# Kernel tuning notes

Hardware: AMD Instinct MI355X
Metric: run time of the kernel (lower is better)

Reference implementation:

```python
import jax, jax.numpy as jnp
import numpy as np


def setup_inputs() -> dict:
    key = jax.random.key(0)
    x = jax.random.normal(key, (8192, 16384), dtype=jnp.float32)
    return {"x": x, "k": 128}


def reference(x, k):
    # TopKActivation: keep top-k values per row, zero the rest.
    B, D = x.shape
    if k >= D:
        return x
    top_vals, top_idx = jax.lax.top_k(x, k)           # [B, k], [B, k]
    rows = jnp.arange(B, dtype=top_idx.dtype)[:, None]  # [B, 1]
    out = jnp.zeros_like(x).at[rows, top_idx].set(top_vals)
    return out
```

## Files before the change

### kernel.cpp

```cpp
#include <hip/hip_runtime.h>


#define DCOLS 16384
#define TPB 256
#define CHUNKS (DCOLS / 4 / TPB)
#define KPT (CHUNKS * 4)

__device__ __forceinline__ unsigned enc_f32(float f) {
    unsigned u = __float_as_uint(f);
    return u ^ ((unsigned)((int)u >> 31) | 0x80000000u);
}

__device__ __forceinline__ float dec_f32(unsigned kk) {
    unsigned u = kk ^ (0x80000000u | ~(unsigned)((int)kk >> 31));
    return __uint_as_float(u);
}

__global__ __launch_bounds__(TPB) void topk_act_kernel(
        const float* __restrict__ x, const int* __restrict__ kptr,
        float* __restrict__ out) {
    const int tid = threadIdx.x;
    const long long row = blockIdx.x;
    const float4* __restrict__ xr = (const float4*)x + row * (DCOLS / 4);
    float4* __restrict__ outr = (float4*)out + row * (DCOLS / 4);

    __shared__ int totals[40];
    __shared__ unsigned short epfx[CHUNKS * TPB];

    if (tid < 40) totals[tid] = 0;

    unsigned key[KPT];
#pragma unroll
    for (int j = 0; j < CHUNKS; ++j) {
        float4 v = xr[j * TPB + tid];
        key[j * 4 + 0] = enc_f32(v.x);
        key[j * 4 + 1] = enc_f32(v.y);
        key[j * 4 + 2] = enc_f32(v.z);
        key[j * 4 + 3] = enc_f32(v.w);
    }
    const int k = *kptr;
    __syncthreads();

    if (k >= DCOLS || k <= 0) {
        const bool keep_all = (k >= DCOLS);
#pragma unroll
        for (int j = 0; j < CHUNKS; ++j) {
            float4 o;
            o.x = keep_all ? dec_f32(key[j * 4 + 0]) : 0.0f;
            o.y = keep_all ? dec_f32(key[j * 4 + 1]) : 0.0f;
            o.z = keep_all ? dec_f32(key[j * 4 + 2]) : 0.0f;
            o.w = keep_all ? dec_f32(key[j * 4 + 3]) : 0.0f;
            outr[j * TPB + tid] = o;
        }
        return;
    }

    unsigned lo = 0u, hi = 0xFFFFFFFFu;
    int it = 0;
    while (lo < hi) {
        const unsigned mid = lo + ((hi - lo) >> 1);
        int cnt = 0;
#pragma unroll
        for (int i = 0; i < KPT; ++i) cnt += (key[i] > mid) ? 1 : 0;
#pragma unroll
        for (int off = 32; off > 0; off >>= 1) cnt += __shfl_xor(cnt, off);
        if ((tid & 63) == 0) atomicAdd(&totals[it], cnt);
        __syncthreads();
        const int f = totals[it];
        if (f < k) hi = mid; else lo = mid + 1;
        ++it;
    }
    const unsigned ts = lo;

    int gc = 0, ec = 0;
    unsigned long long eqmask = 0ull;
#pragma unroll
    for (int i = 0; i < KPT; ++i) {
        gc += (key[i] > ts) ? 1 : 0;
        if (key[i] == ts) { ec += 1; eqmask |= (1ull << i); }
    }
    int gcs = gc, ecs = ec;
#pragma unroll
    for (int off = 32; off > 0; off >>= 1) {
        gcs += __shfl_xor(gcs, off);
        ecs += __shfl_xor(ecs, off);
    }
    if ((tid & 63) == 0) {
        atomicAdd(&totals[36], gcs);
        atomicAdd(&totals[37], ecs);
    }
    __syncthreads();
    const int cntG = totals[36];
    const int cntE = totals[37];
    const int r = k - cntG;

    unsigned long long keepmask = ~0ull;
    if (r != cntE) {
#pragma unroll
        for (int j = 0; j < CHUNKS; ++j) {
            unsigned nib = (unsigned)((eqmask >> (j * 4)) & 0xFull);
            unsigned c4 = (nib & 1u) + ((nib >> 1) & 1u) + ((nib >> 2) & 1u) +
                          ((nib >> 3) & 1u);
            epfx[j * TPB + tid] = (unsigned short)c4;
        }
        __syncthreads();
        if (tid == 0) {
            unsigned run = 0;
            for (int m = 0; m < CHUNKS * TPB; ++m) {
                unsigned v = epfx[m];
                epfx[m] = (unsigned short)run;
                run += v;
            }
        }
        __syncthreads();
        keepmask = 0ull;
#pragma unroll
        for (int j = 0; j < CHUNKS; ++j) {
            int base = (int)epfx[j * TPB + tid];
#pragma unroll
            for (int c = 0; c < 4; ++c) {
                if ((eqmask >> (j * 4 + c)) & 1ull) {
                    if (base < r) keepmask |= (1ull << (j * 4 + c));
                    base += 1;
                }
            }
        }
    }

#pragma unroll
    for (int j = 0; j < CHUNKS; ++j) {
        float4 o;
#pragma unroll
        for (int c = 0; c < 4; ++c) {
            const unsigned kk = key[j * 4 + c];
            const bool keep =
                (kk > ts) || ((kk == ts) && ((keepmask >> (j * 4 + c)) & 1ull));
            ((float*)&o)[c] = keep ? dec_f32(kk) : 0.0f;
        }
        outr[j * TPB + tid] = o;
    }
}

extern "C" void kernel_launch(void* const* d_in, const int* in_sizes, int n_in,
                              void* d_out, int out_size, void* d_ws,
                              size_t ws_size, hipStream_t stream) {
    const float* x = (const float*)d_in[0];
    const int* kp = (const int*)d_in[1];
    float* out = (float*)d_out;
    const int B = in_sizes[0] / DCOLS;
    topk_act_kernel<<<B, TPB, 0, stream>>>(x, kp, out);
}
```

Before: 1.102 ms.

## Replace bitwise binary search with 4-pass 8-bit radix select via shared histograms

Swaps the 32-iteration threshold binary search, which scans all 64 register keys per iteration, for a radix select. Four passes each build a 256-bin histogram of one byte of the key in shared memory, using 32 sub-histogram columns to spread atomic contention. Each pass locates the bin holding the k-th element with a wave-level suffix scan. This cuts the number of full key scans and block barriers, at the cost of many LDS atomics, histogram zeroing, and about 33KB of shared memory per block. It also adds a launch-bounds occupancy hint of 4 blocks per SM.

```diff
diff --git a/kernel.cpp b/kernel.cpp
--- a/kernel.cpp
+++ b/kernel.cpp
@@ -5,6 +5,7 @@
 #define TPB 256
 #define CHUNKS (DCOLS / 4 / TPB)
 #define KPT (CHUNKS * 4)
+#define NSUB 32
 
 __device__ __forceinline__ unsigned enc_f32(float f) {
     unsigned u = __float_as_uint(f);
@@ -16,7 +17,7 @@
     return __uint_as_float(u);
 }
 
-__global__ __launch_bounds__(TPB) void topk_act_kernel(
+__global__ __launch_bounds__(TPB, 4) void topk_act_kernel(
         const float* __restrict__ x, const int* __restrict__ kptr,
         float* __restrict__ out) {
     const int tid = threadIdx.x;
@@ -24,10 +25,15 @@
     const float4* __restrict__ xr = (const float4*)x + row * (DCOLS / 4);
     float4* __restrict__ outr = (float4*)out + row * (DCOLS / 4);
 
-    __shared__ int totals[40];
-    __shared__ unsigned short epfx[CHUNKS * TPB];
-
-    if (tid < 40) totals[tid] = 0;
+    __shared__ __align__(16) unsigned hist[257 * NSUB];
+    __shared__ __align__(16) unsigned bintot[256];
+    __shared__ int meta[4];
+
+    unsigned short* epfx = (unsigned short*)hist;
+
+    uint4* h4 = (uint4*)hist;
+#pragma unroll
+    for (int j = 0; j < 8; ++j) h4[j * TPB + tid] = make_uint4(0u, 0u, 0u, 0u);
 
     unsigned key[KPT];
 #pragma unroll
@@ -55,47 +61,94 @@
         return;
     }
 
-    unsigned lo = 0u, hi = 0xFFFFFFFFu;
-    int it = 0;
-    while (lo < hi) {
-        const unsigned mid = lo + ((hi - lo) >> 1);
-        int cnt = 0;
-#pragma unroll
-        for (int i = 0; i < KPT; ++i) cnt += (key[i] > mid) ? 1 : 0;
-#pragma unroll
-        for (int off = 32; off > 0; off >>= 1) cnt += __shfl_xor(cnt, off);
-        if ((tid & 63) == 0) atomicAdd(&totals[it], cnt);
-        __syncthreads();
-        const int f = totals[it];
-        if (f < k) hi = mid; else lo = mid + 1;
-        ++it;
-    }
-    const unsigned ts = lo;
-
-    int gc = 0, ec = 0;
-    unsigned long long eqmask = 0ull;
-#pragma unroll
-    for (int i = 0; i < KPT; ++i) {
-        gc += (key[i] > ts) ? 1 : 0;
-        if (key[i] == ts) { ec += 1; eqmask |= (1ull << i); }
-    }
-    int gcs = gc, ecs = ec;
-#pragma unroll
-    for (int off = 32; off > 0; off >>= 1) {
-        gcs += __shfl_xor(gcs, off);
-        ecs += __shfl_xor(ecs, off);
-    }
-    if ((tid & 63) == 0) {
-        atomicAdd(&totals[36], gcs);
-        atomicAdd(&totals[37], ecs);
-    }
-    __syncthreads();
-    const int cntG = totals[36];
-    const int cntE = totals[37];
+    const int col = tid & (NSUB - 1);
+
+#pragma unroll
+    for (int i = 0; i < KPT; ++i)
+        atomicAdd(&hist[(key[i] >> 24) * NSUB + col], 1u);
+
+    unsigned prefix = 0u;
+    int base = 0;
+    int cntE = 0;
+
+#pragma unroll
+    for (int pass = 0; pass < 4; ++pass) {
+        const int shift = 24 - 8 * pass;
+        __syncthreads();
+
+        {
+            const unsigned* hb = &hist[tid * NSUB];
+            unsigned s = 0;
+            int idx = tid & (NSUB - 1);
+#pragma unroll
+            for (int c = 0; c < NSUB; ++c) {
+                s += hb[idx];
+                idx = (idx + 1) & (NSUB - 1);
+            }
+            bintot[tid] = s;
+        }
+        __syncthreads();
+
+        if (tid < 64) {
+            const uint4 t4 = ((const uint4*)bintot)[tid];
+            const unsigned s = t4.x + t4.y + t4.z + t4.w;
+            unsigned v = s;
+#pragma unroll
+            for (int off = 1; off < 64; off <<= 1) {
+                unsigned t = __shfl_down(v, off);
+                v += (tid + off < 64) ? t : 0u;
+            }
+            const int lsuf = (int)(v - s);
+            const int need = k - base;
+            const int g3 = lsuf;
+            const int g2 = g3 + (int)t4.w;
+            const int g1 = g2 + (int)t4.z;
+            const int g0 = g1 + (int)t4.y;
+            int d = -1, g = 0, e = 0;
+            if (g3 < need && need <= g2) { d = 4 * tid + 3; g = g3; e = (int)t4.w; }
+            else if (g2 < need && need <= g1) { d = 4 * tid + 2; g = g2; e = (int)t4.z; }
+            else if (g1 < need && need <= g0) { d = 4 * tid + 1; g = g1; e = (int)t4.y; }
+            else if (g0 < need && need <= g0 + (int)t4.x) { d = 4 * tid; g = g0; e = (int)t4.x; }
+            if (d >= 0) {
+                meta[0] = d;
+                meta[1] = base + g;
+                meta[2] = e;
+            }
+        }
+        if (pass < 3) {
+#pragma unroll
+            for (int j = 0; j < 8; ++j)
+                h4[j * TPB + tid] = make_uint4(0u, 0u, 0u, 0u);
+        }
+        __syncthreads();
+
+        prefix |= (unsigned)meta[0] << shift;
+        base = meta[1];
+        cntE = meta[2];
+
+        if (pass < 3) {
+            const int nshift = shift - 8;
+            const unsigned pm = prefix >> shift;
+#pragma unroll
+            for (int i = 0; i < KPT; ++i) {
+                const unsigned b = ((key[i] >> shift) == pm)
+                                       ? ((key[i] >> nshift) & 255u)
+                                       : 256u;
+                atomicAdd(&hist[b * NSUB + col], 1u);
+            }
+        }
+    }
+
+    const unsigned ts = prefix;
+    const int cntG = base;
     const int r = k - cntG;
 
     unsigned long long keepmask = ~0ull;
     if (r != cntE) {
+        unsigned long long eqmask = 0ull;
+#pragma unroll
+        for (int i = 0; i < KPT; ++i)
+            if (key[i] == ts) eqmask |= (1ull << i);
 #pragma unroll
         for (int j = 0; j < CHUNKS; ++j) {
             unsigned nib = (unsigned)((eqmask >> (j * 4)) & 0xFull);
@@ -107,21 +160,21 @@
         if (tid == 0) {
             unsigned run = 0;
             for (int m = 0; m < CHUNKS * TPB; ++m) {
-                unsigned v = epfx[m];
+                unsigned vv = epfx[m];
                 epfx[m] = (unsigned short)run;
-                run += v;
+                run += vv;
             }
         }
         __syncthreads();
         keepmask = 0ull;
 #pragma unroll
         for (int j = 0; j < CHUNKS; ++j) {
-            int base = (int)epfx[j * TPB + tid];
+            int bb = (int)epfx[j * TPB + tid];
 #pragma unroll
             for (int c = 0; c < 4; ++c) {
                 if ((eqmask >> (j * 4 + c)) & 1ull) {
-                    if (base < r) keepmask |= (1ull << (j * 4 + c));
-                    base += 1;
+                    if (bb < r) keepmask |= (1ull << (j * 4 + c));
+                    bb += 1;
                 }
             }
         }
```

New measurement: 899.0 us. 18.4% less time.
